# Performance work log

Hardware: AMD Instinct MI355X
Metric: run time of the kernel (lower is better)

## Reference

```python
import jax, jax.numpy as jnp
import numpy as np

N = 65536      # total nodes
M = 1024       # molecules
C = 128        # c_dim
MD = 256       # m_dim
RADIUS = 2
NEG = -1e9


def _gru_cell(x, h_prev, W_ih, b_ih, W_hh, b_hh):
    # torch GRUCell math. W_ih: [3*MD, C], W_hh: [3*MD, MD]
    gi = x @ W_ih.T + b_ih          # [M, 3*MD]
    gh = h_prev @ W_hh.T + b_hh     # [M, 3*MD]
    i_r, i_z, i_n = jnp.split(gi, 3, axis=-1)
    h_r, h_z, h_n = jnp.split(gh, 3, axis=-1)
    r = jax.nn.sigmoid(i_r + h_r)
    z = jax.nn.sigmoid(i_z + h_z)
    n = jnp.tanh(i_n + r * h_n)
    return (1.0 - z) * n + z * h_prev


def setup_inputs() -> dict:
    key = jax.random.key(0)
    ks = jax.random.split(key, 10)
    s = 0.05
    node_features = jax.random.normal(ks[0], (N, C), jnp.float32)
    # one-hot molecule membership: node i belongs to molecule i % M
    seg = jnp.arange(N) % M
    mol_node_matrix = jax.nn.one_hot(seg, M, dtype=jnp.float32).T  # [M, N]
    mol_node_mask = jnp.where(mol_node_matrix > 0, 0.0, NEG).astype(jnp.float32)
    return {
        "node_features": node_features,
        "mol_node_matrix": mol_node_matrix,
        "mol_node_mask": mol_node_mask,
        "W_map": jax.random.normal(ks[1], (MD, C), jnp.float32) * s,
        "b_map": jnp.zeros((MD,), jnp.float32),
        "W_att": jax.random.normal(ks[2], (C, C), jnp.float32) * s,
        "b_att": jnp.zeros((C,), jnp.float32),
        "W_align": jax.random.normal(ks[3], (1, MD + C), jnp.float32) * s,
        "b_align": jnp.zeros((1,), jnp.float32),
        "W_ih": jax.random.normal(ks[4], (3 * MD, C), jnp.float32) * s,
        "b_ih": jnp.zeros((3 * MD,), jnp.float32),
        "W_hh": jax.random.normal(ks[5], (3 * MD, MD), jnp.float32) * s,
        "b_hh": jnp.zeros((3 * MD,), jnp.float32),
    }


def reference(node_features, mol_node_matrix, mol_node_mask,
              W_map, b_map, W_att, b_att, W_align, b_align,
              W_ih, b_ih, W_hh, b_hh):
    leaky = jax.nn.leaky_relu  # default slope 0.01 matches torch LeakyReLU
    # initial pooled molecule features: [M, MD]
    mol = mol_node_matrix @ leaky(node_features @ W_map.T + b_map)
    for _ in range(RADIUS):
        h = node_features @ W_att.T + b_att                 # [N, C] (dropout p=0)
        pooled = mol_node_matrix.T @ mol                    # [N, MD] broadcast mol->node
        a = leaky(jnp.concatenate([pooled, node_features], axis=-1) @ W_align.T + b_align)  # [N,1]
        # mnm @ diag(a) == column-scale by a
        scores = mol_node_matrix * a[:, 0][None, :] + mol_node_mask  # [M, N]
        w = jax.nn.softmax(scores, axis=1)
        context = jax.nn.elu(w @ h)                         # [M, C]
        mol = jax.nn.relu(_gru_cell(context, mol, W_ih, b_ih, W_hh, b_hh))
    return mol
```

## Files before the change

### kernel.cpp

```cpp
#include <hip/hip_runtime.h>
#include <cstdint>

#define NN 65536
#define MM 1024
#define CC 128
#define MDIM 256

typedef short short8 __attribute__((ext_vector_type(8)));
typedef float f32x4 __attribute__((ext_vector_type(4)));

__device__ __forceinline__ unsigned short f2bf(float f) {
  unsigned int u = __float_as_uint(f);
  unsigned int r = (u + 0x7fffu + ((u >> 16) & 1u)) >> 16;
  return (unsigned short)r;
}
__device__ __forceinline__ float bf2f(unsigned int us) {
  return __uint_as_float(us << 16);
}

__global__ __launch_bounds__(256) void prepare(
    const float* __restrict__ nf, const float* __restrict__ w2,
    const float* __restrict__ b_align, unsigned short* __restrict__ nf_bf,
    float* __restrict__ a_node,
    const float* __restrict__ Wmap, const float* __restrict__ Watt,
    const float* __restrict__ Wih, const float* __restrict__ Whh,
    unsigned short* __restrict__ Wmap_bf, unsigned short* __restrict__ Watt_bf,
    unsigned short* __restrict__ Wih_bf, unsigned short* __restrict__ Whh_bf) {
  const int blk = blockIdx.x;
  const int t = threadIdx.x;
  if (blk < 1024) {
    const int row = blk * 64 + (t >> 2);
    const int c0 = (t & 3) * 32;
    const float* src = nf + (size_t)row * CC + c0;
    unsigned short* dst = nf_bf + (size_t)row * CC + c0;
    float part = 0.0f;
#pragma unroll
    for (int i = 0; i < 32; i += 4) {
      float4 v = *(const float4*)(src + i);
      float4 w = *(const float4*)(w2 + c0 + i);
      part += v.x * w.x + v.y * w.y + v.z * w.z + v.w * w.w;
      ushort4 u;
      u.x = f2bf(v.x); u.y = f2bf(v.y); u.z = f2bf(v.z); u.w = f2bf(v.w);
      *(ushort4*)(dst + i) = u;
    }
    part += __shfl_xor(part, 1);
    part += __shfl_xor(part, 2);
    if ((t & 3) == 0) a_node[row] = part + b_align[0];
  } else {
    int idx = (blk - 1024) * 2048 + t * 8;
    const float* s;
    unsigned short* d;
    if (idx < 32768)       { s = Wmap + idx;          d = Wmap_bf + idx; }
    else if (idx < 49152)  { s = Watt + idx - 32768;  d = Watt_bf + idx - 32768; }
    else if (idx < 147456) { s = Wih + idx - 49152;   d = Wih_bf + idx - 49152; }
    else                   { s = Whh + idx - 147456;  d = Whh_bf + idx - 147456; }
#pragma unroll
    for (int i = 0; i < 8; i += 4) {
      float4 v = *(const float4*)(s + i);
      ushort4 u;
      u.x = f2bf(v.x); u.y = f2bf(v.y); u.z = f2bf(v.z); u.w = f2bf(v.w);
      *(ushort4*)(d + i) = u;
    }
  }
}

__global__ __launch_bounds__(256) void fused_nf(
    const unsigned short* __restrict__ nf_bf,
    const unsigned short* __restrict__ Watt_bf, const float* __restrict__ b_att,
    unsigned short* __restrict__ h_bf,
    const unsigned short* __restrict__ Wmap_bf, const float* __restrict__ bmap,
    float* __restrict__ mol0, unsigned short* __restrict__ mol0_bf) {
  const int t = threadIdx.x;
  const int w = t >> 6, l = t & 63;
  const int lane16 = l & 15, quad = l >> 4;

  if (blockIdx.x < 1024) {
    const int row0 = blockIdx.x * 64;
    f32x4 acc[4][2];
#pragma unroll
    for (int a = 0; a < 4; ++a) {
      acc[a][0] = (f32x4){0.f, 0.f, 0.f, 0.f};
      acc[a][1] = (f32x4){0.f, 0.f, 0.f, 0.f};
    }
#pragma unroll
    for (int ks = 0; ks < 4; ++ks) {
      const int k0 = ks * 32 + quad * 8;
      short8 af[4], bfr[2];
#pragma unroll
      for (int mt = 0; mt < 4; ++mt)
        af[mt] = *(const short8*)(nf_bf + (size_t)(row0 + mt * 16 + lane16) * CC + k0);
#pragma unroll
      for (int nt = 0; nt < 2; ++nt)
        bfr[nt] = *(const short8*)(Watt_bf + (size_t)(w * 32 + nt * 16 + lane16) * CC + k0);
#pragma unroll
      for (int mt = 0; mt < 4; ++mt)
#pragma unroll
        for (int nt = 0; nt < 2; ++nt)
          acc[mt][nt] = __builtin_amdgcn_mfma_f32_16x16x32_bf16(
              af[mt], bfr[nt], acc[mt][nt], 0, 0, 0);
    }
#pragma unroll
    for (int nt = 0; nt < 2; ++nt) {
      const int col = w * 32 + nt * 16 + lane16;
      const float b = b_att[col];
#pragma unroll
      for (int mt = 0; mt < 4; ++mt)
#pragma unroll
        for (int r = 0; r < 4; ++r) {
          const int row = row0 + mt * 16 + quad * 4 + r;
          h_bf[(size_t)row * CC + col] = f2bf(acc[mt][nt][r] + b);
        }
    }
  } else {
    const int m = blockIdx.x - 1024;
    f32x4 acc[4][4];
#pragma unroll
    for (int a = 0; a < 4; ++a)
#pragma unroll
      for (int b = 0; b < 4; ++b) acc[a][b] = (f32x4){0.f, 0.f, 0.f, 0.f};
#pragma unroll
    for (int ks = 0; ks < 4; ++ks) {
      const int k0 = ks * 32 + quad * 8;
      short8 af[4], bfr[4];
#pragma unroll
      for (int mt = 0; mt < 4; ++mt)
        af[mt] = *(const short8*)(nf_bf + (size_t)(m + (mt * 16 + lane16) * MM) * CC + k0);
#pragma unroll
      for (int nt = 0; nt < 4; ++nt)
        bfr[nt] = *(const short8*)(Wmap_bf + (size_t)(w * 64 + nt * 16 + lane16) * CC + k0);
#pragma unroll
      for (int mt = 0; mt < 4; ++mt)
#pragma unroll
        for (int nt = 0; nt < 4; ++nt)
          acc[mt][nt] = __builtin_amdgcn_mfma_f32_16x16x32_bf16(
              af[mt], bfr[nt], acc[mt][nt], 0, 0, 0);
    }
#pragma unroll
    for (int nt = 0; nt < 4; ++nt) {
      const int col = w * 64 + nt * 16 + lane16;
      const float b = bmap[col];
      float s = 0.0f;
#pragma unroll
      for (int mt = 0; mt < 4; ++mt)
#pragma unroll
        for (int r = 0; r < 4; ++r) {
          float v = acc[mt][nt][r] + b;
          s += (v > 0.0f) ? v : 0.01f * v;
        }
      s += __shfl_xor(s, 16);
      s += __shfl_xor(s, 32);
      if (quad == 0) {
        mol0[(size_t)m * MDIM + col] = s;
        mol0_bf[(size_t)m * MDIM + col] = f2bf(s);
      }
    }
  }
}

__global__ __launch_bounds__(256) void attend(
    const unsigned short* __restrict__ h_bf, const float* __restrict__ a_node,
    const float* __restrict__ mol, const float* __restrict__ w1,
    unsigned short* __restrict__ ctx_bf) {
  const int m = blockIdx.x;
  const int t = threadIdx.x;
  const int w = t >> 6, l = t & 63;
  __shared__ float red[4][128];

  float4 mv = *(const float4*)(mol + (size_t)m * MDIM + l * 4);
  float4 wv = *(const float4*)(w1 + l * 4);
  float molp = mv.x * wv.x + mv.y * wv.y + mv.z * wv.z + mv.w * wv.w;
#pragma unroll
  for (int off = 32; off; off >>= 1) molp += __shfl_xor(molp, off);
  float a = a_node[m + l * MM] + molp;
  a = a > 0.0f ? a : 0.01f * a;
  float mx = a;
#pragma unroll
  for (int off = 32; off; off >>= 1) mx = fmaxf(mx, __shfl_xor(mx, off));
  float e = __expf(a - mx);
  float s = e;
#pragma unroll
  for (int off = 32; off; off >>= 1) s += __shfl_xor(s, off);
  const float wl = e / s;

  float a0 = 0.f, a1 = 0.f;
#pragma unroll
  for (int jj = 0; jj < 16; ++jj) {
    const int j = w * 16 + jj;
    float wj = __shfl(wl, j);
    unsigned int u = *(const unsigned int*)(h_bf + (size_t)(m + j * MM) * CC + 2 * l);
    a0 = fmaf(wj, bf2f(u & 0xffffu), a0);
    a1 = fmaf(wj, bf2f(u >> 16), a1);
  }
  red[w][2 * l]     = a0;
  red[w][2 * l + 1] = a1;
  __syncthreads();
  if (w == 0) {
    float b0 = red[0][2 * l]     + red[1][2 * l]     + red[2][2 * l]     + red[3][2 * l];
    float b1 = red[0][2 * l + 1] + red[1][2 * l + 1] + red[2][2 * l + 1] + red[3][2 * l + 1];
    float o0 = b0 > 0.f ? b0 : (__expf(b0) - 1.0f);
    float o1 = b1 > 0.f ? b1 : (__expf(b1) - 1.0f);
    unsigned int pack = (unsigned int)f2bf(o0) | ((unsigned int)f2bf(o1) << 16);
    *(unsigned int*)(ctx_bf + (size_t)m * CC + 2 * l) = pack;
  }
}

__global__ __launch_bounds__(256) void gru_fused(
    const unsigned short* __restrict__ ctx_bf,
    const float* __restrict__ molprev, const unsigned short* __restrict__ molprev_bf,
    const unsigned short* __restrict__ Wih_bf, const unsigned short* __restrict__ Whh_bf,
    const float* __restrict__ b_ih, const float* __restrict__ b_hh,
    float* __restrict__ out_f32, unsigned short* __restrict__ out_bf) {
  const int t = threadIdx.x;
  const int w = t >> 6, l = t & 63;
  const int lane16 = l & 15, quad = l >> 4;
  const int d0 = blockIdx.x * 16;
  const int m0 = blockIdx.y * 64;
  const int rw = m0 + w * 16 + lane16;

  f32x4 acc_i[3], acc_h[3];
#pragma unroll
  for (int i = 0; i < 3; ++i) {
    acc_i[i] = (f32x4){0.f, 0.f, 0.f, 0.f};
    acc_h[i] = (f32x4){0.f, 0.f, 0.f, 0.f};
  }

#pragma unroll
  for (int ks = 0; ks < 4; ++ks) {
    const int k0 = ks * 32 + quad * 8;
    short8 af = *(const short8*)(ctx_bf + (size_t)rw * CC + k0);
#pragma unroll
    for (int nt = 0; nt < 3; ++nt) {
      const int brow = nt * 256 + d0 + lane16;
      short8 bfr = *(const short8*)(Wih_bf + (size_t)brow * CC + k0);
      acc_i[nt] = __builtin_amdgcn_mfma_f32_16x16x32_bf16(af, bfr, acc_i[nt], 0, 0, 0);
    }
  }
#pragma unroll
  for (int ks = 0; ks < 8; ++ks) {
    const int k0 = ks * 32 + quad * 8;
    short8 af = *(const short8*)(molprev_bf + (size_t)rw * MDIM + k0);
#pragma unroll
    for (int nt = 0; nt < 3; ++nt) {
      const int brow = nt * 256 + d0 + lane16;
      short8 bfr = *(const short8*)(Whh_bf + (size_t)brow * MDIM + k0);
      acc_h[nt] = __builtin_amdgcn_mfma_f32_16x16x32_bf16(af, bfr, acc_h[nt], 0, 0, 0);
    }
  }

  {
    const int d = d0 + lane16;
    const float bir = b_ih[d],       bhr = b_hh[d];
    const float biz = b_ih[d + 256], bhz = b_hh[d + 256];
    const float bin = b_ih[d + 512], bhn = b_hh[d + 512];
#pragma unroll
    for (int r = 0; r < 4; ++r) {
      const int row = m0 + w * 16 + quad * 4 + r;
      float ir = acc_i[0][r] + bir, hr = acc_h[0][r] + bhr;
      float iz = acc_i[1][r] + biz, hz = acc_h[1][r] + bhz;
      float in = acc_i[2][r] + bin, hn = acc_h[2][r] + bhn;
      float rg = 1.0f / (1.0f + __expf(-(ir + hr)));
      float z  = 1.0f / (1.0f + __expf(-(iz + hz)));
      float n  = tanhf(in + rg * hn);
      float hp = molprev[(size_t)row * MDIM + d];
      float v = (1.0f - z) * n + z * hp;
      v = v > 0.0f ? v : 0.0f;
      out_f32[(size_t)row * MDIM + d] = v;
      if (out_bf) out_bf[(size_t)row * MDIM + d] = f2bf(v);
    }
  }
}

extern "C" void kernel_launch(void* const* d_in, const int* in_sizes, int n_in,
                              void* d_out, int out_size, void* d_ws, size_t ws_size,
                              hipStream_t stream) {
  const float* nf      = (const float*)d_in[0];
  const float* W_map   = (const float*)d_in[3];
  const float* b_map   = (const float*)d_in[4];
  const float* W_att   = (const float*)d_in[5];
  const float* b_att   = (const float*)d_in[6];
  const float* W_align = (const float*)d_in[7];
  const float* b_align = (const float*)d_in[8];
  const float* W_ih    = (const float*)d_in[9];
  const float* b_ih    = (const float*)d_in[10];
  const float* W_hh    = (const float*)d_in[11];
  const float* b_hh    = (const float*)d_in[12];
  float* outp = (float*)d_out;

  float* ws = (float*)d_ws;
  unsigned short* nf_bf    = (unsigned short*)ws; ws += (size_t)NN * CC / 2;
  unsigned short* h_bf     = (unsigned short*)ws; ws += (size_t)NN * CC / 2;
  unsigned short* Wmap_bf  = (unsigned short*)ws; ws += MDIM * CC / 2;
  unsigned short* Watt_bf  = (unsigned short*)ws; ws += CC * CC / 2;
  unsigned short* Wih_bf   = (unsigned short*)ws; ws += 768 * CC / 2;
  unsigned short* Whh_bf   = (unsigned short*)ws; ws += 768 * MDIM / 2;
  unsigned short* ctx_bf   = (unsigned short*)ws; ws += (size_t)MM * CC / 2;
  unsigned short* molA_bf  = (unsigned short*)ws; ws += (size_t)MM * MDIM / 2;
  unsigned short* molB_bf  = (unsigned short*)ws; ws += (size_t)MM * MDIM / 2;
  float* a_node = ws; ws += NN;
  float* mol_a  = ws; ws += (size_t)MM * MDIM;
  float* mol_b  = ws; ws += (size_t)MM * MDIM;

  prepare<<<dim3(1192), 256, 0, stream>>>(nf, W_align + MDIM, b_align, nf_bf,
                                          a_node, W_map, W_att, W_ih, W_hh,
                                          Wmap_bf, Watt_bf, Wih_bf, Whh_bf);
  fused_nf<<<dim3(2048), 256, 0, stream>>>(nf_bf, Watt_bf, b_att, h_bf,
                                           Wmap_bf, b_map, mol_a, molA_bf);

  attend<<<dim3(1024), 256, 0, stream>>>(h_bf, a_node, mol_a, W_align, ctx_bf);
  gru_fused<<<dim3(16, 16), 256, 0, stream>>>(ctx_bf, mol_a, molA_bf,
                                              Wih_bf, Whh_bf, b_ih, b_hh,
                                              mol_b, molB_bf);
  attend<<<dim3(1024), 256, 0, stream>>>(h_bf, a_node, mol_b, W_align, ctx_bf);
  gru_fused<<<dim3(16, 16), 256, 0, stream>>>(ctx_bf, mol_b, molB_bf,
                                              Wih_bf, Whh_bf, b_ih, b_hh,
                                              outp, (unsigned short*)nullptr);
}
```

Baseline: 497.8 us.

## Fuse node bf16 conversion into per-molecule GEMM block via swizzled LDS tile

The node-feature bf16 conversion and align-score dot product move from the prepare kernel into the node GEMM kernel. Each block now handles the 64 nodes of one molecule, stages them as bf16 in an XOR-swizzled shared-memory tile, and reuses that tile for both the W_att and W_map MFMA products. h is stored molecule-major, so the attend kernel reads it contiguously. This removes the global nf_bf round trip and the duplicate strided reads, at the cost of fewer, heavier blocks and strided fp32 loads of node_features.

```diff
diff --git a/kernel.cpp b/kernel.cpp
--- a/kernel.cpp
+++ b/kernel.cpp
@@ -18,64 +18,67 @@
   return __uint_as_float(us << 16);
 }
 
-__global__ __launch_bounds__(256) void prepare(
-    const float* __restrict__ nf, const float* __restrict__ w2,
-    const float* __restrict__ b_align, unsigned short* __restrict__ nf_bf,
-    float* __restrict__ a_node,
+__global__ __launch_bounds__(256) void convert_w(
     const float* __restrict__ Wmap, const float* __restrict__ Watt,
     const float* __restrict__ Wih, const float* __restrict__ Whh,
     unsigned short* __restrict__ Wmap_bf, unsigned short* __restrict__ Watt_bf,
     unsigned short* __restrict__ Wih_bf, unsigned short* __restrict__ Whh_bf) {
-  const int blk = blockIdx.x;
-  const int t = threadIdx.x;
-  if (blk < 1024) {
-    const int row = blk * 64 + (t >> 2);
-    const int c0 = (t & 3) * 32;
-    const float* src = nf + (size_t)row * CC + c0;
-    unsigned short* dst = nf_bf + (size_t)row * CC + c0;
-    float part = 0.0f;
-#pragma unroll
-    for (int i = 0; i < 32; i += 4) {
-      float4 v = *(const float4*)(src + i);
-      float4 w = *(const float4*)(w2 + c0 + i);
-      part += v.x * w.x + v.y * w.y + v.z * w.z + v.w * w.w;
-      ushort4 u;
-      u.x = f2bf(v.x); u.y = f2bf(v.y); u.z = f2bf(v.z); u.w = f2bf(v.w);
-      *(ushort4*)(dst + i) = u;
-    }
-    part += __shfl_xor(part, 1);
-    part += __shfl_xor(part, 2);
-    if ((t & 3) == 0) a_node[row] = part + b_align[0];
-  } else {
-    int idx = (blk - 1024) * 2048 + t * 8;
-    const float* s;
-    unsigned short* d;
-    if (idx < 32768)       { s = Wmap + idx;          d = Wmap_bf + idx; }
-    else if (idx < 49152)  { s = Watt + idx - 32768;  d = Watt_bf + idx - 32768; }
-    else if (idx < 147456) { s = Wih + idx - 49152;   d = Wih_bf + idx - 49152; }
-    else                   { s = Whh + idx - 147456;  d = Whh_bf + idx - 147456; }
-#pragma unroll
-    for (int i = 0; i < 8; i += 4) {
-      float4 v = *(const float4*)(s + i);
-      ushort4 u;
-      u.x = f2bf(v.x); u.y = f2bf(v.y); u.z = f2bf(v.z); u.w = f2bf(v.w);
-      *(ushort4*)(d + i) = u;
-    }
-  }
-}
-
-__global__ __launch_bounds__(256) void fused_nf(
-    const unsigned short* __restrict__ nf_bf,
+  int idx = blockIdx.x * 2048 + threadIdx.x * 8;
+  const float* s;
+  unsigned short* d;
+  if (idx < 32768)       { s = Wmap + idx;          d = Wmap_bf + idx; }
+  else if (idx < 49152)  { s = Watt + idx - 32768;  d = Watt_bf + idx - 32768; }
+  else if (idx < 147456) { s = Wih + idx - 49152;   d = Wih_bf + idx - 49152; }
+  else                   { s = Whh + idx - 147456;  d = Whh_bf + idx - 147456; }
+#pragma unroll
+  for (int i = 0; i < 8; i += 4) {
+    float4 v = *(const float4*)(s + i);
+    ushort4 u;
+    u.x = f2bf(v.x); u.y = f2bf(v.y); u.z = f2bf(v.z); u.w = f2bf(v.w);
+    *(ushort4*)(d + i) = u;
+  }
+}
+
+__global__ __launch_bounds__(256) void node_fused(
+    const float* __restrict__ nf, const float* __restrict__ w2,
+    const float* __restrict__ b_align,
     const unsigned short* __restrict__ Watt_bf, const float* __restrict__ b_att,
-    unsigned short* __restrict__ h_bf,
     const unsigned short* __restrict__ Wmap_bf, const float* __restrict__ bmap,
+    unsigned short* __restrict__ h_bf, float* __restrict__ a_node,
     float* __restrict__ mol0, unsigned short* __restrict__ mol0_bf) {
+  const int m = blockIdx.x;
   const int t = threadIdx.x;
   const int w = t >> 6, l = t & 63;
   const int lane16 = l & 15, quad = l >> 4;
-
-  if (blockIdx.x < 1024) {
-    const int row0 = blockIdx.x * 64;
+  __shared__ unsigned short Abf[64 * 128];
+
+  {
+    const int j = t >> 2;
+    const int c0 = (t & 3) * 32;
+    const float* src = nf + (size_t)(m + j * MM) * CC + c0;
+    float part = 0.0f;
+#pragma unroll
+    for (int i = 0; i < 32; i += 4) {
+      float4 v = *(const float4*)(src + i);
+      float4 wv = *(const float4*)(w2 + c0 + i);
+      part += v.x * wv.x + v.y * wv.y + v.z * wv.z + v.w * wv.w;
+      ushort4 u;
+      u.x = f2bf(v.x); u.y = f2bf(v.y); u.z = f2bf(v.z); u.w = f2bf(v.w);
+      unsigned int byt = (unsigned int)(j * 256 + (c0 + i) * 2) ^ ((unsigned int)(j & 7) << 4);
+      *(ushort4*)((char*)Abf + byt) = u;
+    }
+    part += __shfl_xor(part, 1);
+    part += __shfl_xor(part, 2);
+    if ((t & 3) == 0) a_node[m + j * MM] = part + b_align[0];
+  }
+  __syncthreads();
+
+#define LDA(row, k0)                                                        \
+  (*(const short8*)((const char*)Abf +                                      \
+                    (((unsigned int)((row) * 256 + (k0) * 2)) ^             \
+                     ((unsigned int)((row) & 7) << 4))))
+
+  {
     f32x4 acc[4][2];
 #pragma unroll
     for (int a = 0; a < 4; ++a) {
@@ -87,8 +90,7 @@
       const int k0 = ks * 32 + quad * 8;
       short8 af[4], bfr[2];
 #pragma unroll
-      for (int mt = 0; mt < 4; ++mt)
-        af[mt] = *(const short8*)(nf_bf + (size_t)(row0 + mt * 16 + lane16) * CC + k0);
+      for (int mt = 0; mt < 4; ++mt) af[mt] = LDA(mt * 16 + lane16, k0);
 #pragma unroll
       for (int nt = 0; nt < 2; ++nt)
         bfr[nt] = *(const short8*)(Watt_bf + (size_t)(w * 32 + nt * 16 + lane16) * CC + k0);
@@ -107,12 +109,13 @@
       for (int mt = 0; mt < 4; ++mt)
 #pragma unroll
         for (int r = 0; r < 4; ++r) {
-          const int row = row0 + mt * 16 + quad * 4 + r;
-          h_bf[(size_t)row * CC + col] = f2bf(acc[mt][nt][r] + b);
+          const int j = mt * 16 + quad * 4 + r;
+          h_bf[(size_t)(m * 64 + j) * CC + col] = f2bf(acc[mt][nt][r] + b);
         }
     }
-  } else {
-    const int m = blockIdx.x - 1024;
+  }
+
+  {
     f32x4 acc[4][4];
 #pragma unroll
     for (int a = 0; a < 4; ++a)
@@ -123,8 +126,7 @@
       const int k0 = ks * 32 + quad * 8;
       short8 af[4], bfr[4];
 #pragma unroll
-      for (int mt = 0; mt < 4; ++mt)
-        af[mt] = *(const short8*)(nf_bf + (size_t)(m + (mt * 16 + lane16) * MM) * CC + k0);
+      for (int mt = 0; mt < 4; ++mt) af[mt] = LDA(mt * 16 + lane16, k0);
 #pragma unroll
       for (int nt = 0; nt < 4; ++nt)
         bfr[nt] = *(const short8*)(Wmap_bf + (size_t)(w * 64 + nt * 16 + lane16) * CC + k0);
@@ -155,6 +157,7 @@
       }
     }
   }
+#undef LDA
 }
 
 __global__ __launch_bounds__(256) void attend(
@@ -187,7 +190,7 @@
   for (int jj = 0; jj < 16; ++jj) {
     const int j = w * 16 + jj;
     float wj = __shfl(wl, j);
-    unsigned int u = *(const unsigned int*)(h_bf + (size_t)(m + j * MM) * CC + 2 * l);
+    unsigned int u = *(const unsigned int*)(h_bf + (size_t)(m * 64 + j) * CC + 2 * l);
     a0 = fmaf(wj, bf2f(u & 0xffffu), a0);
     a1 = fmaf(wj, bf2f(u >> 16), a1);
   }
@@ -287,7 +290,6 @@
   float* outp = (float*)d_out;
 
   float* ws = (float*)d_ws;
-  unsigned short* nf_bf    = (unsigned short*)ws; ws += (size_t)NN * CC / 2;
   unsigned short* h_bf     = (unsigned short*)ws; ws += (size_t)NN * CC / 2;
   unsigned short* Wmap_bf  = (unsigned short*)ws; ws += MDIM * CC / 2;
   unsigned short* Watt_bf  = (unsigned short*)ws; ws += CC * CC / 2;
@@ -300,11 +302,11 @@
   float* mol_a  = ws; ws += (size_t)MM * MDIM;
   float* mol_b  = ws; ws += (size_t)MM * MDIM;
 
-  prepare<<<dim3(1192), 256, 0, stream>>>(nf, W_align + MDIM, b_align, nf_bf,
-                                          a_node, W_map, W_att, W_ih, W_hh,
-                                          Wmap_bf, Watt_bf, Wih_bf, Whh_bf);
-  fused_nf<<<dim3(2048), 256, 0, stream>>>(nf_bf, Watt_bf, b_att, h_bf,
-                                           Wmap_bf, b_map, mol_a, molA_bf);
+  convert_w<<<dim3(168), 256, 0, stream>>>(W_map, W_att, W_ih, W_hh,
+                                           Wmap_bf, Watt_bf, Wih_bf, Whh_bf);
+  node_fused<<<dim3(1024), 256, 0, stream>>>(nf, W_align + MDIM, b_align,
+                                             Watt_bf, b_att, Wmap_bf, b_map,
+                                             h_bf, a_node, mol_a, molA_bf);
 
   attend<<<dim3(1024), 256, 0, stream>>>(h_bf, a_node, mol_a, W_align, ctx_bf);
   gru_fused<<<dim3(16, 16), 256, 0, stream>>>(ctx_bf, mol_a, molA_bf,
```

After: 481.2 us. 3.3% less time.
